# Performance work log

Measured on AMD Instinct MI355X. Metric: run time of the kernel, lower is better.

Reference implementation:

```python
import jax, jax.numpy as jnp
import numpy as np

D_IN = 4096
NUM_HEADS = 32
NUM_KV_GROUPS = 8
HEAD_DIM = D_IN // NUM_HEADS  # 128 (init overwrites head_dim)
GROUP_SIZE = NUM_HEADS // NUM_KV_GROUPS
SEQ = 2048
BATCH = 1
EPS = 1e-6


def layernorm(t, w, b):
    mu = jnp.mean(t, axis=-1, keepdims=True)
    var = jnp.var(t, axis=-1, keepdims=True)
    return (t - mu) * jax.lax.rsqrt(var + EPS) * w + b


def rope(t, cos, sin):
    # t: [B, H, S, D]; cos/sin: [S, D] broadcast over B, H
    half = t.shape[-1] // 2
    x1, x2 = t[..., :half], t[..., half:]
    rot = jnp.concatenate([-x2, x1], axis=-1)
    return t * cos + rot * sin


def setup_inputs() -> dict:
    key = jax.random.key(0)
    ks = jax.random.split(key, 10)
    x = jax.random.normal(ks[0], (BATCH, SEQ, D_IN), dtype=jnp.float32)
    mask = jnp.triu(jnp.ones((SEQ, SEQ), dtype=bool), k=1)  # True = masked (causal)
    # RoPE tables
    inv_freq = 1.0 / (10000.0 ** (np.arange(0, HEAD_DIM, 2, dtype=np.float32) / HEAD_DIM))
    pos = np.arange(SEQ, dtype=np.float32)
    ang = np.einsum('s,d->sd', pos, inv_freq)  # [S, D/2]
    ang = np.concatenate([ang, ang], axis=-1)  # [S, D]
    cos = jnp.asarray(np.cos(ang))
    sin = jnp.asarray(np.sin(ang))
    s = 0.02
    Wq = jax.random.normal(ks[1], (D_IN, NUM_HEADS * HEAD_DIM), dtype=jnp.float32) * s
    Wk = jax.random.normal(ks[2], (D_IN, NUM_KV_GROUPS * HEAD_DIM), dtype=jnp.float32) * s
    Wv = jax.random.normal(ks[3], (D_IN, NUM_KV_GROUPS * HEAD_DIM), dtype=jnp.float32) * s
    Wo = jax.random.normal(ks[4], (NUM_HEADS * HEAD_DIM, D_IN), dtype=jnp.float32) * s
    qn_w = jnp.ones((HEAD_DIM,), jnp.float32)
    qn_b = jnp.zeros((HEAD_DIM,), jnp.float32)
    kn_w = jnp.ones((HEAD_DIM,), jnp.float32)
    kn_b = jnp.zeros((HEAD_DIM,), jnp.float32)
    return {"x": x, "mask": mask, "cos": cos, "sin": sin, "Wq": Wq, "Wk": Wk,
            "Wv": Wv, "Wo": Wo, "qn_w": qn_w, "qn_b": qn_b, "kn_w": kn_w, "kn_b": kn_b}


def reference(x, mask, cos, sin, Wq, Wk, Wv, Wo, qn_w, qn_b, kn_w, kn_b):
    B, S, _ = x.shape
    q = (x @ Wq).reshape(B, S, NUM_HEADS, HEAD_DIM).transpose(0, 2, 1, 3)      # [B,H,S,D]
    k = (x @ Wk).reshape(B, S, NUM_KV_GROUPS, HEAD_DIM).transpose(0, 2, 1, 3)  # [B,G,S,D]
    v = (x @ Wv).reshape(B, S, NUM_KV_GROUPS, HEAD_DIM).transpose(0, 2, 1, 3)
    q = layernorm(q, qn_w, qn_b)
    k = layernorm(k, kn_w, kn_b)
    q = rope(q, cos, sin)
    k = rope(k, cos, sin)
    k = jnp.repeat(k, GROUP_SIZE, axis=1)  # [B,H,S,D]
    v = jnp.repeat(v, GROUP_SIZE, axis=1)
    scores = jnp.einsum('bhqd,bhkd->bhqk', q, k)
    scores = jnp.where(mask, -jnp.inf, scores)
    attn = jax.nn.softmax(scores / jnp.sqrt(jnp.float32(HEAD_DIM)), axis=-1)
    ctx = jnp.einsum('bhqk,bhkd->bhqd', attn, v)
    ctx = ctx.transpose(0, 2, 1, 3).reshape(B, S, NUM_HEADS * HEAD_DIM)
    return ctx @ Wo
```

## Files before the change

### kernel.cpp

```cpp
#include <hip/hip_runtime.h>
#include <stdint.h>

#define SQ   2048
#define DIN  4096
#define NH   32
#define NKV  8
#define HD   128
#define NQKV 6144

typedef float f32x4 __attribute__((ext_vector_type(4)));
typedef short bf16x8 __attribute__((ext_vector_type(8)));

__device__ __forceinline__ short f2bf(float f) {
  union { float f; uint32_t u; } v; v.f = f;
  uint32_t r = (v.u + 0x7FFFu + ((v.u >> 16) & 1u)) >> 16;
  return (short)r;
}

__device__ __forceinline__ void gl2lds(const void* g, void* l) {
  __builtin_amdgcn_global_load_lds(
      (const __attribute__((address_space(1))) void*)g,
      (__attribute__((address_space(3))) void*)l, 16, 0, 0);
}

__global__ void cvt_bf16(const float* __restrict__ src, short* __restrict__ dst, long n) {
  long i = ((long)blockIdx.x * blockDim.x + threadIdx.x) * 4;
  if (i + 3 < n) {
    float4 v = *(const float4*)(src + i);
    short o[4] = { f2bf(v.x), f2bf(v.y), f2bf(v.z), f2bf(v.w) };
    *(uint2*)(dst + i) = *(uint2*)o;
  }
}

__global__ __launch_bounds__(256) void transpose_cvt(const float* __restrict__ src, int ldS, long zS,
                                                     short* __restrict__ dst, int ldD, long zD) {
  __shared__ float tile[64][65];
  src += (long)blockIdx.z * zS;
  dst += (long)blockIdx.z * zD;
  int r0 = blockIdx.y * 64, c0 = blockIdx.x * 64;
  int tid = threadIdx.x;
#pragma unroll
  for (int i = 0; i < 16; ++i) {
    int idx = i * 256 + tid;
    int rr = idx >> 6, cc = idx & 63;
    tile[rr][cc] = src[(long)(r0 + rr) * ldS + c0 + cc];
  }
  __syncthreads();
#pragma unroll
  for (int i = 0; i < 16; ++i) {
    int idx = i * 256 + tid;
    int dr = idx >> 6, dc = idx & 63;
    dst[(long)(c0 + dr) * ldD + r0 + dc] = f2bf(tile[dc][dr]);
  }
}

#define ASZ   16384
#define BUFSZ 32768
#define MFMA(d, a, b) d = __builtin_amdgcn_mfma_f32_16x16x32_bf16(a, b, d, 0, 0, 0)

#define SA(t) { short* d = &lds[(((t) & 1) * BUFSZ) + dA]; const short* s = aS + (long)(t) * 64; \
                gl2lds(s, d); gl2lds(s + K8, d + 512); gl2lds(s + 2 * K8, d + 1024); gl2lds(s + 3 * K8, d + 1536); }
#define SB(t) { short* d = &lds[(((t) & 1) * BUFSZ) + dB]; const short* s = bS + (long)(t) * 64; \
                gl2lds(s, d); gl2lds(s + K8, d + 512); gl2lds(s + 2 * K8, d + 1024); gl2lds(s + 3 * K8, d + 1536); }

__global__ __launch_bounds__(512, 2) void gemm8p(const short* __restrict__ A, const short* __restrict__ Bt,
                                                 float* __restrict__ C, int M, int N, int K) {
  __shared__ __align__(16) short lds[2 * BUFSZ];
  int nwg = gridDim.x;
  int lin = ((int)blockIdx.x & 7) * (nwg >> 3) + ((int)blockIdx.x >> 3);
  int mt = M >> 8;
  int m0 = (lin % mt) << 8, n0 = (lin / mt) << 8;

  int tid = threadIdx.x;
  int w = tid >> 6, lane = tid & 63;
  int l16 = lane & 15, lq = lane >> 4;
  int wm = (w >> 2) << 7;
  int wn = (w & 3) << 6;

  int s7 = l16 & 7;
  int fo0 = ((lq ^ s7) << 3);
  int fo1 = (((lq + 4) ^ s7) << 3);
  int arow = (wm + l16) * 64;
  int brow = ASZ + (wn + l16) * 64;

  int srow = lane >> 3;
  int gch = (lane & 7) ^ srow;
  const short* aS = A + (long)(m0 + 32 * w + srow) * K + gch * 8;
  const short* bS = Bt + (long)(n0 + 32 * w + srow) * K + gch * 8;
  long K8 = 8L * K;
  int dA = (32 * w) * 64;
  int dB = ASZ + (32 * w) * 64;

  f32x4 acc[8][4] = {};
  const int KT = K >> 6;

  SA(0); SB(0);
  asm volatile("s_waitcnt vmcnt(0)" ::: "memory");
  __builtin_amdgcn_s_barrier();

  for (int t = 0; t < KT; ++t) {
    const short* buf = &lds[(t & 1) * BUFSZ];
    bool s1 = (t + 1 < KT);
    bf16x8 af[8], b0, b1;

#pragma unroll
    for (int i = 0; i < 8; ++i) af[i] = *(const bf16x8*)&buf[arow + i * 1024 + fo0];
    b0 = *(const bf16x8*)&buf[brow + fo0];
    b1 = *(const bf16x8*)&buf[brow + 1024 + fo0];
    if (s1) SA(t + 1);
    __builtin_amdgcn_s_barrier();
    asm volatile("s_waitcnt lgkmcnt(0)" ::: "memory");
    __builtin_amdgcn_s_setprio(1);
#pragma unroll
    for (int i = 0; i < 8; ++i) { MFMA(acc[i][0], af[i], b0); MFMA(acc[i][1], af[i], b1); }
    __builtin_amdgcn_s_setprio(0);
    __builtin_amdgcn_s_barrier();

    b0 = *(const bf16x8*)&buf[brow + 2048 + fo0];
    b1 = *(const bf16x8*)&buf[brow + 3072 + fo0];
    if (s1) SB(t + 1);
    __builtin_amdgcn_s_barrier();
    asm volatile("s_waitcnt lgkmcnt(0)" ::: "memory");
    __builtin_amdgcn_s_setprio(1);
#pragma unroll
    for (int i = 0; i < 8; ++i) { MFMA(acc[i][2], af[i], b0); MFMA(acc[i][3], af[i], b1); }
    __builtin_amdgcn_s_setprio(0);
    __builtin_amdgcn_s_barrier();

#pragma unroll
    for (int i = 0; i < 8; ++i) af[i] = *(const bf16x8*)&buf[arow + i * 1024 + fo1];
    b0 = *(const bf16x8*)&buf[brow + 2048 + fo1];
    b1 = *(const bf16x8*)&buf[brow + 3072 + fo1];
    __builtin_amdgcn_s_barrier();
    asm volatile("s_waitcnt lgkmcnt(0)" ::: "memory");
    __builtin_amdgcn_s_setprio(1);
#pragma unroll
    for (int i = 0; i < 8; ++i) { MFMA(acc[i][2], af[i], b0); MFMA(acc[i][3], af[i], b1); }
    __builtin_amdgcn_s_setprio(0);
    __builtin_amdgcn_s_barrier();

    b0 = *(const bf16x8*)&buf[brow + fo1];
    b1 = *(const bf16x8*)&buf[brow + 1024 + fo1];
    __builtin_amdgcn_s_barrier();
    asm volatile("s_waitcnt lgkmcnt(0)" ::: "memory");
    __builtin_amdgcn_s_setprio(1);
#pragma unroll
    for (int i = 0; i < 8; ++i) { MFMA(acc[i][0], af[i], b0); MFMA(acc[i][1], af[i], b1); }
    __builtin_amdgcn_s_setprio(0);
    if (s1) {
      asm volatile("s_waitcnt vmcnt(0)" ::: "memory");
      __builtin_amdgcn_s_barrier();
    }
  }

#pragma unroll
  for (int i = 0; i < 8; ++i)
#pragma unroll
    for (int j = 0; j < 4; ++j)
#pragma unroll
      for (int r = 0; r < 4; ++r)
        C[(long)(m0 + wm + i * 16 + lq * 4 + r) * N + n0 + wn + j * 16 + l16] = acc[i][j][r];
}

__global__ __launch_bounds__(64) void ln_rope(const float* __restrict__ qkv,
                                              const float* __restrict__ cosb, const float* __restrict__ sinb,
                                              const float* __restrict__ qw, const float* __restrict__ qb,
                                              const float* __restrict__ kw, const float* __restrict__ kb,
                                              short* __restrict__ qo, short* __restrict__ ko) {
  int s = blockIdx.x, slice = blockIdx.y, t = threadIdx.x;
  bool isq = slice < NH;
  int off = isq ? slice * HD : DIN + (slice - NH) * HD;
  const float* src = qkv + (long)s * NQKV + off;
  float v0 = src[t], v1 = src[t + 64];
  float sum = v0 + v1, ss = v0 * v0 + v1 * v1;
#pragma unroll
  for (int o = 1; o < 64; o <<= 1) { sum += __shfl_xor(sum, o); ss += __shfl_xor(ss, o); }
  float mu = sum * (1.f / 128.f);
  float var = ss * (1.f / 128.f) - mu * mu;
  float rstd = rsqrtf(var + 1e-6f);
  const float* w  = isq ? qw : kw;
  const float* bb = isq ? qb : kb;
  float n0 = (v0 - mu) * rstd * w[t]      + bb[t];
  float n1 = (v1 - mu) * rstd * w[t + 64] + bb[t + 64];
  float c0 = cosb[s * HD + t], c1 = cosb[s * HD + t + 64];
  float s0 = sinb[s * HD + t], s1 = sinb[s * HD + t + 64];
  float o0 = n0 * c0 - n1 * s0;
  float o1 = n1 * c1 + n0 * s1;
  short* dst = isq ? (qo + ((long)slice * SQ + s) * HD)
                   : (ko + ((long)(slice - NH) * SQ + s) * HD);
  dst[t] = f2bf(o0);
  dst[t + 64] = f2bf(o1);
}

__global__ __launch_bounds__(256) void attn(const short* __restrict__ q, const short* __restrict__ k,
                                            const short* __restrict__ vT, short* __restrict__ ctx) {
  int pair = blockIdx.x, h = blockIdx.y, g = h >> 2;
  int tid = threadIdx.x, w = tid >> 6, lane = tid & 63;
  int l16 = lane & 15, lq = lane >> 4;
  __shared__ __align__(16) short Ks[64 * 128];
  __shared__ __align__(16) short Vs[128 * 64];
  __shared__ __align__(16) short pbuf[4][16 * 72];
  const short* qh = q + (long)h * SQ * HD;
  const short* kg = k + (long)g * SQ * HD;
  const short* vg = vT + (long)g * HD * SQ;
  int kr = (w * 4) * 4 + (lane >> 4);
  int vrw = (w * 4) * 8 + (lane >> 3);
  const float sc = 0.08838834764831845f * 1.4426950408889634f;

  for (int st = 0; st < 2; ++st) {
    int qt = st ? (31 - pair) : pair;
    int qbase = qt * 64 + w * 16;
    bf16x8 aq[4];
#pragma unroll
    for (int kk = 0; kk < 4; ++kk)
      aq[kk] = *(const bf16x8*)&qh[(long)(qbase + l16) * HD + kk * 32 + lq * 8];
    float m_r[4], l_r[4];
    f32x4 acc[8] = {};
#pragma unroll
    for (int r = 0; r < 4; ++r) { m_r[r] = -__builtin_inff(); l_r[r] = 0.f; }

    for (int kt = 0; kt <= qt; ++kt) {
#pragma unroll
      for (int j = 0; j < 4; ++j) {
        int call = w * 4 + j;
        int r = kr + j * 4;
        int chk = (lane & 15) ^ (r & 15);
        gl2lds(&kg[(long)(kt * 64 + r) * HD + chk * 8], &Ks[call * 512]);
        int rv = vrw + j * 8;
        int chv = (lane & 7) ^ (rv & 7);
        gl2lds(&vg[(long)rv * SQ + kt * 64 + chv * 8], &Vs[call * 512]);
      }
      __syncthreads();
      f32x4 s4[4];
#pragma unroll
      for (int b = 0; b < 4; ++b) s4[b] = (f32x4){0.f, 0.f, 0.f, 0.f};
#pragma unroll
      for (int b = 0; b < 4; ++b) {
        int krow = b * 16 + l16;
#pragma unroll
        for (int kk = 0; kk < 4; ++kk) {
          bf16x8 bk = *(const bf16x8*)&Ks[krow * 128 + ((kk * 4 + lq) ^ (krow & 15)) * 8];
          s4[b] = __builtin_amdgcn_mfma_f32_16x16x32_bf16(aq[kk], bk, s4[b], 0, 0, 0);
        }
      }
      int qrow0 = qbase + lq * 4;
#pragma unroll
      for (int b = 0; b < 4; ++b) {
        int key = kt * 64 + b * 16 + l16;
#pragma unroll
        for (int r = 0; r < 4; ++r) {
          float val = s4[b][r] * sc;
          s4[b][r] = (key > qrow0 + r) ? -__builtin_inff() : val;
        }
      }
      float p[4][4];
#pragma unroll
      for (int r = 0; r < 4; ++r) {
        float mx = fmaxf(fmaxf(s4[0][r], s4[1][r]), fmaxf(s4[2][r], s4[3][r]));
#pragma unroll
        for (int o = 1; o < 16; o <<= 1) mx = fmaxf(mx, __shfl_xor(mx, o));
        float mnew = fmaxf(m_r[r], mx);
        float alpha = exp2f(m_r[r] - mnew);
        float sum = 0.f;
#pragma unroll
        for (int b = 0; b < 4; ++b) { float pv = exp2f(s4[b][r] - mnew); p[b][r] = pv; sum += pv; }
#pragma unroll
        for (int o = 1; o < 16; o <<= 1) sum += __shfl_xor(sum, o);
        l_r[r] = l_r[r] * alpha + sum;
        m_r[r] = mnew;
#pragma unroll
        for (int n = 0; n < 8; ++n) acc[n][r] *= alpha;
      }
#pragma unroll
      for (int b = 0; b < 4; ++b)
#pragma unroll
        for (int r = 0; r < 4; ++r)
          pbuf[w][(lq * 4 + r) * 72 + b * 16 + l16] = f2bf(p[b][r]);
#pragma unroll
      for (int kk = 0; kk < 2; ++kk) {
        bf16x8 pf = *(const bf16x8*)&pbuf[w][l16 * 72 + kk * 32 + lq * 8];
#pragma unroll
        for (int n = 0; n < 8; ++n) {
          int vrow = n * 16 + l16;
          bf16x8 vf = *(const bf16x8*)&Vs[vrow * 64 + ((kk * 4 + lq) ^ (vrow & 7)) * 8];
          acc[n] = __builtin_amdgcn_mfma_f32_16x16x32_bf16(pf, vf, acc[n], 0, 0, 0);
        }
      }
      __syncthreads();
    }
#pragma unroll
    for (int n = 0; n < 8; ++n)
#pragma unroll
      for (int r = 0; r < 4; ++r) {
        int srow = qbase + lq * 4 + r;
        ctx[(long)srow * (NH * HD) + h * HD + n * 16 + l16] = f2bf(acc[n][r] / l_r[r]);
      }
  }
}

#define XB_OFF     0L
#define QR_OFF     0L
#define WQKVT_OFF  16777216L
#define KR_OFF     16777216L
#define VT_OFF     20971520L
#define CTX_OFF    25165824L
#define WOT_OFF    67108864L
#define QKV_OFF    100663296L

extern "C" void kernel_launch(void* const* d_in, const int* in_sizes, int n_in,
                              void* d_out, int out_size, void* d_ws, size_t ws_size,
                              hipStream_t stream) {
  const float* x    = (const float*)d_in[0];
  const float* cosb = (const float*)d_in[2];
  const float* sinb = (const float*)d_in[3];
  const float* Wq   = (const float*)d_in[4];
  const float* Wk   = (const float*)d_in[5];
  const float* Wv   = (const float*)d_in[6];
  const float* Wo   = (const float*)d_in[7];
  const float* qnw  = (const float*)d_in[8];
  const float* qnb  = (const float*)d_in[9];
  const float* knw  = (const float*)d_in[10];
  const float* knb  = (const float*)d_in[11];

  char* ws = (char*)d_ws;
  short* xb    = (short*)(ws + XB_OFF);
  short* qr    = (short*)(ws + QR_OFF);
  short* wqkvt = (short*)(ws + WQKVT_OFF);
  short* krp   = (short*)(ws + KR_OFF);
  short* vt    = (short*)(ws + VT_OFF);
  short* ctx   = (short*)(ws + CTX_OFF);
  short* wot   = (short*)(ws + WOT_OFF);
  float* qkv   = (float*)(ws + QKV_OFF);

  cvt_bf16<<<8192, 256, 0, stream>>>(x, xb, (long)SQ * DIN);
  transpose_cvt<<<dim3(64, 64, 1), 256, 0, stream>>>(Wq, 4096, 0L, wqkvt, 4096, 0L);
  transpose_cvt<<<dim3(16, 64, 1), 256, 0, stream>>>(Wk, 1024, 0L, wqkvt + (long)4096 * 4096, 4096, 0L);
  transpose_cvt<<<dim3(16, 64, 1), 256, 0, stream>>>(Wv, 1024, 0L, wqkvt + (long)5120 * 4096, 4096, 0L);
  transpose_cvt<<<dim3(64, 64, 1), 256, 0, stream>>>(Wo, 4096, 0L, wot, 4096, 0L);
  gemm8p<<<(SQ / 256) * (NQKV / 256), 512, 0, stream>>>(xb, wqkvt, qkv, SQ, NQKV, DIN);
  ln_rope<<<dim3(SQ, NH + NKV), 64, 0, stream>>>(qkv, cosb, sinb, qnw, qnb, knw, knb, qr, krp);
  transpose_cvt<<<dim3(2, 32, 8), 256, 0, stream>>>(qkv + 5120, NQKV, 128L, vt, SQ, (long)HD * SQ);
  attn<<<dim3(16, NH), 256, 0, stream>>>(qr, krp, vt, ctx);
  gemm8p<<<(SQ / 256) * (DIN / 256), 512, 0, stream>>>(ctx, wot, (float*)d_out, SQ, DIN, DIN);
}
```

Before: 598.4 us.

## Double-buffer K/V tiles in attention, mask only diagonal tile, defer softmax rescale

The attention kernel now double-buffers its K and V shared-memory tiles. It issues the global-to-LDS loads for the next key tile before computing on the current one, waits with explicit vmcnt counts, and uses bare s_barrier in place of __syncthreads. The causal mask is applied only on the diagonal tile; off-diagonal tiles just scale the scores. Online-softmax rescaling of the accumulators is skipped when no row's max grows by more than 8 in log2 space. This trades extra LDS use, which may lower occupancy, and hand-written waitcnt logic for overlap of memory loads with MFMA work and fewer per-tile VALU operations.

```diff
diff --git a/kernel.cpp b/kernel.cpp
--- a/kernel.cpp
+++ b/kernel.cpp
@@ -197,8 +197,8 @@
   int pair = blockIdx.x, h = blockIdx.y, g = h >> 2;
   int tid = threadIdx.x, w = tid >> 6, lane = tid & 63;
   int l16 = lane & 15, lq = lane >> 4;
-  __shared__ __align__(16) short Ks[64 * 128];
-  __shared__ __align__(16) short Vs[128 * 64];
+  __shared__ __align__(16) short Ks[2][64 * 128];
+  __shared__ __align__(16) short Vs[2][128 * 64];
   __shared__ __align__(16) short pbuf[4][16 * 72];
   const short* qh = q + (long)h * SQ * HD;
   const short* kg = k + (long)g * SQ * HD;
@@ -219,18 +219,37 @@
 #pragma unroll
     for (int r = 0; r < 4; ++r) { m_r[r] = -__builtin_inff(); l_r[r] = 0.f; }
 
+#pragma unroll
+    for (int j = 0; j < 4; ++j) {
+      int call = w * 4 + j;
+      int r = kr + j * 4;
+      int chk = (lane & 15) ^ (r & 15);
+      gl2lds(&kg[(long)r * HD + chk * 8], &Ks[0][call * 512]);
+      int rv = vrw + j * 8;
+      int chv = (lane & 7) ^ (rv & 7);
+      gl2lds(&vg[(long)rv * SQ + chv * 8], &Vs[0][call * 512]);
+    }
+
     for (int kt = 0; kt <= qt; ++kt) {
-#pragma unroll
-      for (int j = 0; j < 4; ++j) {
-        int call = w * 4 + j;
-        int r = kr + j * 4;
-        int chk = (lane & 15) ^ (r & 15);
-        gl2lds(&kg[(long)(kt * 64 + r) * HD + chk * 8], &Ks[call * 512]);
-        int rv = vrw + j * 8;
-        int chv = (lane & 7) ^ (rv & 7);
-        gl2lds(&vg[(long)rv * SQ + kt * 64 + chv * 8], &Vs[call * 512]);
-      }
-      __syncthreads();
+      int cur = kt & 1;
+      bool more = kt < qt;
+      if (more) {
+#pragma unroll
+        for (int j = 0; j < 4; ++j) {
+          int call = w * 4 + j;
+          int r = kr + j * 4;
+          int chk = (lane & 15) ^ (r & 15);
+          gl2lds(&kg[(long)((kt + 1) * 64 + r) * HD + chk * 8], &Ks[cur ^ 1][call * 512]);
+          int rv = vrw + j * 8;
+          int chv = (lane & 7) ^ (rv & 7);
+          gl2lds(&vg[(long)rv * SQ + (kt + 1) * 64 + chv * 8], &Vs[cur ^ 1][call * 512]);
+        }
+        asm volatile("s_waitcnt vmcnt(8)" ::: "memory");
+      } else {
+        asm volatile("s_waitcnt vmcnt(0)" ::: "memory");
+      }
+      __builtin_amdgcn_s_barrier();
+
       f32x4 s4[4];
 #pragma unroll
       for (int b = 0; b < 4; ++b) s4[b] = (f32x4){0.f, 0.f, 0.f, 0.f};
@@ -239,37 +258,57 @@
         int krow = b * 16 + l16;
 #pragma unroll
         for (int kk = 0; kk < 4; ++kk) {
-          bf16x8 bk = *(const bf16x8*)&Ks[krow * 128 + ((kk * 4 + lq) ^ (krow & 15)) * 8];
+          bf16x8 bk = *(const bf16x8*)&Ks[cur][krow * 128 + ((kk * 4 + lq) ^ (krow & 15)) * 8];
           s4[b] = __builtin_amdgcn_mfma_f32_16x16x32_bf16(aq[kk], bk, s4[b], 0, 0, 0);
         }
       }
       int qrow0 = qbase + lq * 4;
-#pragma unroll
-      for (int b = 0; b < 4; ++b) {
-        int key = kt * 64 + b * 16 + l16;
-#pragma unroll
-        for (int r = 0; r < 4; ++r) {
-          float val = s4[b][r] * sc;
-          s4[b][r] = (key > qrow0 + r) ? -__builtin_inff() : val;
-        }
-      }
-      float p[4][4];
+      if (kt == qt) {
+#pragma unroll
+        for (int b = 0; b < 4; ++b) {
+          int key = kt * 64 + b * 16 + l16;
+#pragma unroll
+          for (int r = 0; r < 4; ++r) {
+            float val = s4[b][r] * sc;
+            s4[b][r] = (key > qrow0 + r) ? -__builtin_inff() : val;
+          }
+        }
+      } else {
+#pragma unroll
+        for (int b = 0; b < 4; ++b)
+#pragma unroll
+          for (int r = 0; r < 4; ++r) s4[b][r] *= sc;
+      }
+      float mx4[4];
+      bool defer = true;
 #pragma unroll
       for (int r = 0; r < 4; ++r) {
         float mx = fmaxf(fmaxf(s4[0][r], s4[1][r]), fmaxf(s4[2][r], s4[3][r]));
 #pragma unroll
         for (int o = 1; o < 16; o <<= 1) mx = fmaxf(mx, __shfl_xor(mx, o));
-        float mnew = fmaxf(m_r[r], mx);
-        float alpha = exp2f(m_r[r] - mnew);
+        mx4[r] = mx;
+        defer = defer && (mx - m_r[r] <= 8.f);
+      }
+      if (!__all((int)defer)) {
+#pragma unroll
+        for (int r = 0; r < 4; ++r) {
+          float mnew = fmaxf(m_r[r], mx4[r]);
+          float alpha = exp2f(m_r[r] - mnew);
+          l_r[r] *= alpha;
+          m_r[r] = mnew;
+#pragma unroll
+          for (int n = 0; n < 8; ++n) acc[n][r] *= alpha;
+        }
+      }
+      float p[4][4];
+#pragma unroll
+      for (int r = 0; r < 4; ++r) {
         float sum = 0.f;
 #pragma unroll
-        for (int b = 0; b < 4; ++b) { float pv = exp2f(s4[b][r] - mnew); p[b][r] = pv; sum += pv; }
+        for (int b = 0; b < 4; ++b) { float pv = exp2f(s4[b][r] - m_r[r]); p[b][r] = pv; sum += pv; }
 #pragma unroll
         for (int o = 1; o < 16; o <<= 1) sum += __shfl_xor(sum, o);
-        l_r[r] = l_r[r] * alpha + sum;
-        m_r[r] = mnew;
-#pragma unroll
-        for (int n = 0; n < 8; ++n) acc[n][r] *= alpha;
+        l_r[r] += sum;
       }
 #pragma unroll
       for (int b = 0; b < 4; ++b)
@@ -282,11 +321,11 @@
 #pragma unroll
         for (int n = 0; n < 8; ++n) {
           int vrow = n * 16 + l16;
-          bf16x8 vf = *(const bf16x8*)&Vs[vrow * 64 + ((kk * 4 + lq) ^ (vrow & 7)) * 8];
+          bf16x8 vf = *(const bf16x8*)&Vs[cur][vrow * 64 + ((kk * 4 + lq) ^ (vrow & 7)) * 8];
           acc[n] = __builtin_amdgcn_mfma_f32_16x16x32_bf16(pf, vf, acc[n], 0, 0, 0);
         }
       }
-      __syncthreads();
+      __builtin_amdgcn_s_barrier();
     }
 #pragma unroll
     for (int n = 0; n < 8; ++n)
```

Result: no change. 591.2 us (-1.2%).
